# Kernel optimization log

Hardware: AMD Instinct MI355X
Metric: run time of the kernel (lower is better)

The kernel has to match this reference:

```python
import jax, jax.numpy as jnp
import numpy as np

D_MODEL = 1024
D_STATE = 128
SEQ_LEN = 4096
BATCH = 4
N_FFT = 2 ** int(np.ceil(np.log2(2 * SEQ_LEN - 1)))  # 8192
LN_EPS = 1e-3  # keras LayerNormalization default epsilon


def setup_inputs() -> dict:
    key = jax.random.key(0)
    ks = jax.random.split(key, 12)
    def dense_w(k, fan_in, fan_out):
        lim = np.sqrt(6.0 / (fan_in + fan_out)).astype(np.float32)  # glorot uniform
        return jax.random.uniform(k, (fan_in, fan_out), jnp.float32, -lim, lim)
    return {
        "x": jax.random.normal(ks[0], (BATCH, SEQ_LEN, D_MODEL), jnp.float32),
        "ln_gamma": jnp.ones((D_MODEL,), jnp.float32),
        "ln_beta": jnp.zeros((D_MODEL,), jnp.float32),
        "W_in": dense_w(ks[1], D_MODEL, D_MODEL),
        "b_in": jnp.zeros((D_MODEL,), jnp.float32),
        "W_xs": dense_w(ks[2], D_MODEL, D_STATE),
        "W_B": dense_w(ks[3], D_MODEL, D_STATE),
        "b_B": jnp.zeros((D_STATE,), jnp.float32),
        "W_C": dense_w(ks[4], D_MODEL, D_STATE),
        "b_C": jnp.zeros((D_STATE,), jnp.float32),
        "A_log": jax.random.uniform(ks[5], (D_STATE,), jnp.float32, -4.0, -1.0),
        "D": jnp.ones((D_MODEL,), jnp.float32),
        "W_so": dense_w(ks[6], D_STATE, D_MODEL),
        "W_out": dense_w(ks[7], D_MODEL, D_MODEL),
        "b_out": jnp.zeros((D_MODEL,), jnp.float32),
    }


def reference(x, ln_gamma, ln_beta, W_in, b_in, W_xs, W_B, b_B, W_C, b_C,
              A_log, D, W_so, W_out, b_out):
    residual = x
    # LayerNorm over last dim
    mu = jnp.mean(x, axis=-1, keepdims=True)
    var = jnp.mean(jnp.square(x - mu), axis=-1, keepdims=True)
    xn = (x - mu) * jax.lax.rsqrt(var + LN_EPS) * ln_gamma + ln_beta
    # projections
    z = xn @ W_in + b_in                      # [B, L, d_model]
    x_state = z @ W_xs                        # [B, L, d_state]
    B_sel = z @ W_B + b_B                     # [B, L, d_state]
    C_sel = z @ W_C + b_C                     # [B, L, d_state]
    # stable A-parameterization -> kernel K[t, s] = exp(A_s * t)
    A = -jnp.exp(A_log)                       # [d_state]
    t = jnp.arange(SEQ_LEN, dtype=jnp.float32)
    K = jnp.exp(t[:, None] * A[None, :])      # [L, d_state]
    # FFT convolution along time axis (zero-padded to N_FFT, causal slice)
    u = x_state * B_sel                       # [B, L, d_state]
    u_f = jnp.fft.rfft(u, n=N_FFT, axis=1)    # [B, N_FFT//2+1, d_state]
    k_f = jnp.fft.rfft(K, n=N_FFT, axis=0)    # [N_FFT//2+1, d_state]
    y_state = jnp.fft.irfft(u_f * k_f[None], n=N_FFT, axis=1)[:, :SEQ_LEN]
    y_state = y_state * C_sel
    # output path with skip connection through D
    y = y_state @ W_so + D * z                # [B, L, d_model]
    y = y @ W_out + b_out
    return y + residual
```

## Files before the change

### kernel.cpp

```cpp
#include <hip/hip_runtime.h>
#include <math.h>

#define D_MODEL 1024
#define D_STATE 128
#define SEQ_LEN 4096
#define BATCH 4
#define NTOK (BATCH * SEQ_LEN)
#define LN_EPS 1e-3f
#define NCHUNK 128
#define LCHUNK (SEQ_LEN / NCHUNK)

typedef __attribute__((ext_vector_type(8))) short bf16x8;
typedef __attribute__((ext_vector_type(4))) float f32x4;

__device__ __forceinline__ short f2bf(float f) {
    union { float f; unsigned u; } v; v.f = f;
    unsigned r = v.u + 0x7FFFu + ((v.u >> 16) & 1u);
    return (short)(r >> 16);
}
__device__ __forceinline__ float bf2f(short s) {
    union { unsigned u; float f; } v; v.u = ((unsigned)(unsigned short)s) << 16;
    return v.f;
}

__global__ __launch_bounds__(256) void ln_kernel(const float* __restrict__ x,
                                                 const float* __restrict__ gamma,
                                                 const float* __restrict__ beta,
                                                 short* __restrict__ xn_bf) {
    int row = blockIdx.x;
    const float4* xr = (const float4*)(x + (size_t)row * D_MODEL);
    float4 v = xr[threadIdx.x];
    float s1 = v.x + v.y + v.z + v.w;
    float s2 = v.x * v.x + v.y * v.y + v.z * v.z + v.w * v.w;
    for (int off = 32; off; off >>= 1) {
        s1 += __shfl_down(s1, off);
        s2 += __shfl_down(s2, off);
    }
    __shared__ float ls1[4], ls2[4];
    int wid = threadIdx.x >> 6, lane = threadIdx.x & 63;
    if (lane == 0) { ls1[wid] = s1; ls2[wid] = s2; }
    __syncthreads();
    s1 = ls1[0] + ls1[1] + ls1[2] + ls1[3];
    s2 = ls2[0] + ls2[1] + ls2[2] + ls2[3];
    float mu = s1 * (1.0f / D_MODEL);
    float var = s2 * (1.0f / D_MODEL) - mu * mu;
    float r = rsqrtf(var + LN_EPS);
    float4 g = ((const float4*)gamma)[threadIdx.x];
    float4 b = ((const float4*)beta)[threadIdx.x];
    short4 o;
    o.x = f2bf((v.x - mu) * r * g.x + b.x);
    o.y = f2bf((v.y - mu) * r * g.y + b.y);
    o.z = f2bf((v.z - mu) * r * g.z + b.z);
    o.w = f2bf((v.w - mu) * r * g.w + b.w);
    ((short4*)(xn_bf + (size_t)row * D_MODEL))[threadIdx.x] = o;
}

__global__ __launch_bounds__(256) void prep_kernel(
    const float* __restrict__ W_in, const float* __restrict__ W_xs,
    const float* __restrict__ W_B, const float* __restrict__ W_C,
    const float* __restrict__ W_so, const float* __restrict__ W_out,
    const float* __restrict__ bB, const float* __restrict__ bC,
    short* __restrict__ W_inT, short* __restrict__ W3T,
    short* __restrict__ W_soT, short* __restrict__ W_outT,
    float* __restrict__ bias3) {
    int blk = blockIdx.x;
    const float* in; short* out; int K, N, tile;
    if (blk < 1024)      { in = W_in;  out = W_inT;           K = 1024; N = 1024; tile = blk; }
    else if (blk < 1152) { in = W_xs;  out = W3T;             K = 1024; N = 128;  tile = blk - 1024; }
    else if (blk < 1280) { in = W_B;   out = W3T + 128*1024;  K = 1024; N = 128;  tile = blk - 1152; }
    else if (blk < 1408) { in = W_C;   out = W3T + 256*1024;  K = 1024; N = 128;  tile = blk - 1280; }
    else if (blk < 1536) { in = W_so;  out = W_soT;           K = 128;  N = 1024; tile = blk - 1408; }
    else if (blk < 2560) { in = W_out; out = W_outT;          K = 1024; N = 1024; tile = blk - 1536; }
    else {
        int t = threadIdx.y * 32 + threadIdx.x;
        for (int n = t; n < 384; n += 256)
            bias3[n] = (n < 128) ? 0.f : ((n < 256) ? bB[n - 128] : bC[n - 256]);
        return;
    }
    __shared__ float t32[32][33];
    int ntiles = N / 32;
    int nb = (tile % ntiles) * 32, kb = (tile / ntiles) * 32;
    int tx = threadIdx.x, ty = threadIdx.y;
#pragma unroll
    for (int i = 0; i < 4; ++i)
        t32[ty + 8 * i][tx] = in[(size_t)(kb + ty + 8 * i) * N + nb + tx];
    __syncthreads();
#pragma unroll
    for (int i = 0; i < 4; ++i)
        out[(size_t)(nb + ty + 8 * i) * K + kb + tx] = f2bf(t32[tx][ty + 8 * i]);
}

template<int HAS_BIAS, int HAS_ADD, int ADD_BF, int HAS_SCALE, int OUT_F32, int OUT_BF, int SWZ>
__global__ __launch_bounds__(256, 4) void gemm_bf16(
    const short* __restrict__ A, const short* __restrict__ BT,
    const float* __restrict__ bias,
    const float* __restrict__ addf, const short* __restrict__ addb,
    const float* __restrict__ addscale,
    float* __restrict__ Cf, short* __restrict__ Cbf,
    int Mt, int Nt, int K) {
    __shared__ short As[128 * 64];
    __shared__ short Bs[128 * 64];
    int p = blockIdx.x;
    int mtile, ntile;
    if (SWZ) {
        int k = p & 7, q = p >> 3;
        ntile = q & 7;
        mtile = k + 8 * (q >> 3);
    } else {
        mtile = p % Mt;
        ntile = p / Mt;
    }
    int m0 = mtile * 128, n0 = ntile * 128;
    int N = Nt * 128;
    int tid = threadIdx.x;
    int lane = tid & 63;
    int w = tid >> 6;
    int quad = lane >> 4, r16 = lane & 15;
    int wm = (w & 1) * 64, wn = (w >> 1) * 64;

    f32x4 acc[4][4] = {};

    for (int k0 = 0; k0 < K; k0 += 64) {
#pragma unroll
        for (int it = 0; it < 4; ++it) {
            int seg = it * 256 + tid;
            int row = seg >> 3, slot = seg & 7;
            int kc8 = slot ^ (row & 7);
            const short* gp = A + (size_t)(m0 + row) * K + k0 + kc8 * 8;
            __builtin_amdgcn_global_load_lds(
                (const __attribute__((address_space(1))) unsigned*)gp,
                (__attribute__((address_space(3))) unsigned*)(As + seg * 8), 16, 0, 0);
        }
#pragma unroll
        for (int it = 0; it < 4; ++it) {
            int seg = it * 256 + tid;
            int row = seg >> 3, slot = seg & 7;
            int kc8 = slot ^ (row & 7);
            const short* gp = BT + (size_t)(n0 + row) * K + k0 + kc8 * 8;
            __builtin_amdgcn_global_load_lds(
                (const __attribute__((address_space(1))) unsigned*)gp,
                (__attribute__((address_space(3))) unsigned*)(Bs + seg * 8), 16, 0, 0);
        }
        __syncthreads();

        const short* abase = As + (wm + r16) * 64;
        const short* bbase = Bs + (wn + r16) * 64;
        int sw = r16 & 7;
#pragma unroll
        for (int kk = 0; kk < 2; ++kk) {
            int phys = ((quad + 4 * kk) ^ sw) * 8;
            bf16x8 af[4], bfr[4];
#pragma unroll
            for (int i = 0; i < 4; ++i) af[i] = *(const bf16x8*)(abase + i * 16 * 64 + phys);
#pragma unroll
            for (int j = 0; j < 4; ++j) bfr[j] = *(const bf16x8*)(bbase + j * 16 * 64 + phys);
#pragma unroll
            for (int i = 0; i < 4; ++i)
#pragma unroll
                for (int j = 0; j < 4; ++j)
                    acc[i][j] = __builtin_amdgcn_mfma_f32_16x16x32_bf16(af[i], bfr[j], acc[i][j], 0, 0, 0);
        }
        __syncthreads();
    }

#pragma unroll
    for (int i = 0; i < 4; ++i) {
#pragma unroll
        for (int j = 0; j < 4; ++j) {
            int col = n0 + wn + j * 16 + r16;
            float bv = HAS_BIAS ? bias[col] : 0.f;
            float sc = HAS_SCALE ? addscale[col] : 1.f;
#pragma unroll
            for (int pr = 0; pr < 4; ++pr) {
                int row = m0 + wm + i * 16 + quad * 4 + pr;
                float v = acc[i][j][pr] + bv;
                if (HAS_ADD) {
                    float av = ADD_BF ? bf2f(addb[(size_t)row * N + col])
                                      : addf[(size_t)row * N + col];
                    v += sc * av;
                }
                if (OUT_F32) Cf[(size_t)row * N + col] = v;
                if (OUT_BF) Cbf[(size_t)row * N + col] = f2bf(v);
            }
        }
    }
}

#define WAITV8 asm volatile("s_waitcnt vmcnt(8)" ::: "memory")
#define WAITV4 asm volatile("s_waitcnt vmcnt(4)" ::: "memory")
#define WAITV0 asm volatile("s_waitcnt vmcnt(0)" ::: "memory")
#define SBARF  do { __builtin_amdgcn_s_barrier(); asm volatile("" ::: "memory"); } while (0)

template<int HAS_BIAS, int HAS_ADD, int OUT_F32, int OUT_BF, int SWZ>
__global__ __launch_bounds__(512, 2) void gemm256(
    const short* __restrict__ A, const short* __restrict__ BT,
    const float* __restrict__ bias, const float* __restrict__ addf,
    float* __restrict__ Cf, short* __restrict__ Cbf,
    int Mt, int Nt, int K) {
    __shared__ short LA[2][2][8192];
    __shared__ short LB[2][2][8192];
    int p = blockIdx.x;
    int mtile, ntile;
    if (SWZ) {
        int xcd = p & 7, q = p >> 3;
        ntile = q % Nt;
        mtile = xcd + 8 * (q / Nt);
    } else {
        mtile = p % Mt;
        ntile = p / Mt;
    }
    int m0 = mtile * 256, n0 = ntile * 256;
    int N = Nt * 256;
    int tid = threadIdx.x;
    int lane = tid & 63, w = tid >> 6;
    int quad = lane >> 4, r16 = lane & 15;
    int wm = w & 1, wn = w >> 1;
    int nt = K >> 6;

    f32x4 acc[8][4] = {};

#define STG(TU, KK, ISB) do { \
        const short* g_ = (ISB) ? BT : A; \
        int rb_ = (ISB) ? n0 : m0; \
        short* l_ = (ISB) ? &LB[(TU) & 1][KK][0] : &LA[(TU) & 1][KK][0]; \
        _Pragma("unroll") \
        for (int r_ = 0; r_ < 2; ++r_) { \
            int seg_ = r_ * 512 + tid; \
            int row_ = seg_ >> 2, sl_ = seg_ & 3; \
            int kc_ = sl_ ^ ((row_ >> 1) & 3); \
            const short* gp_ = g_ + (size_t)(rb_ + row_) * K + (TU) * 64 + (KK) * 32 + kc_ * 8; \
            __builtin_amdgcn_global_load_lds( \
                (const __attribute__((address_space(1))) unsigned*)gp_, \
                (__attribute__((address_space(3))) unsigned*)(&l_[seg_ * 8]), 16, 0, 0); \
        } \
    } while (0)

#define PH_LOADB(Bb) { _Pragma("unroll") for (int j_ = 0; j_ < 4; ++j_) \
        bf[j_] = *(const bf16x8*)((Bb) + j_ * 512 + ph4); }
#define PH_LOADA(Ab, IH) { _Pragma("unroll") for (int i_ = 0; i_ < 4; ++i_) \
        af[i_] = *(const bf16x8*)((Ab) + (i_ + 4 * (IH)) * 512 + ph4); }
#define PH_MFMA(IH) { __builtin_amdgcn_s_setprio(1); \
        _Pragma("unroll") for (int i_ = 0; i_ < 4; ++i_) \
        _Pragma("unroll") for (int j_ = 0; j_ < 4; ++j_) \
            acc[i_ + 4 * (IH)][j_] = __builtin_amdgcn_mfma_f32_16x16x32_bf16( \
                af[i_], bf[j_], acc[i_ + 4 * (IH)][j_], 0, 0, 0); \
        __builtin_amdgcn_s_setprio(0); }

    STG(0, 0, 0); STG(0, 0, 1); STG(0, 1, 0); STG(0, 1, 1); STG(1, 0, 0);

    int ph4 = (quad ^ ((r16 >> 1) & 3)) * 8;
    int arow = (wm << 7) + r16;
    int brow = (wn << 6) + r16;
    bf16x8 af[4], bf[4];

    for (int t = 0; t + 1 < nt; ++t) {
        int c = t & 1;
        const short* Ab0 = &LA[c][0][arow * 32];
        const short* Bb0 = &LB[c][0][brow * 32];
        const short* Ab1 = &LA[c][1][arow * 32];
        const short* Bb1 = &LB[c][1][brow * 32];
        STG(t + 1, 0, 1);
        WAITV8; SBARF;
        PH_LOADB(Bb0); PH_LOADA(Ab0, 0); PH_MFMA(0);
        STG(t + 1, 1, 0);
        WAITV8; SBARF;
        PH_LOADA(Ab0, 1); PH_MFMA(1);
        STG(t + 1, 1, 1);
        WAITV8; SBARF;
        PH_LOADB(Bb1); PH_LOADA(Ab1, 0); PH_MFMA(0);
        if (t + 2 < nt) STG(t + 2, 0, 0);
        WAITV8; SBARF;
        PH_LOADA(Ab1, 1); PH_MFMA(1);
    }
    {
        int c = (nt - 1) & 1;
        const short* Ab0 = &LA[c][0][arow * 32];
        const short* Bb0 = &LB[c][0][brow * 32];
        const short* Ab1 = &LA[c][1][arow * 32];
        const short* Bb1 = &LB[c][1][brow * 32];
        WAITV4; SBARF;
        PH_LOADB(Bb0); PH_LOADA(Ab0, 0); PH_MFMA(0);
        PH_LOADA(Ab0, 1); PH_MFMA(1);
        WAITV0; SBARF;
        PH_LOADB(Bb1); PH_LOADA(Ab1, 0); PH_MFMA(0);
        PH_LOADA(Ab1, 1); PH_MFMA(1);
    }
#undef STG
#undef PH_LOADB
#undef PH_LOADA
#undef PH_MFMA

#pragma unroll
    for (int i = 0; i < 8; ++i) {
#pragma unroll
        for (int j = 0; j < 4; ++j) {
            int col = n0 + wn * 64 + j * 16 + r16;
            float bv = HAS_BIAS ? bias[col] : 0.f;
#pragma unroll
            for (int pr = 0; pr < 4; ++pr) {
                int row = m0 + wm * 128 + i * 16 + quad * 4 + pr;
                float v = acc[i][j][pr] + bv;
                if (HAS_ADD) v += addf[(size_t)row * N + col];
                if (OUT_F32) Cf[(size_t)row * N + col] = v;
                if (OUT_BF) Cbf[(size_t)row * N + col] = f2bf(v);
            }
        }
    }
}

__global__ __launch_bounds__(128) void scan_p1(const float* __restrict__ s3,
                                               const float* __restrict__ A_log,
                                               float* __restrict__ hbuf,
                                               float* __restrict__ Ebuf) {
    int s = threadIdx.x;
    int c = blockIdx.x, b = blockIdx.y;
    float a = expf(-expf(A_log[s]));
    float h = 0.f;
    size_t base = (size_t)b * SEQ_LEN + (size_t)c * LCHUNK;
#pragma unroll 8
    for (int i = 0; i < LCHUNK; ++i) {
        size_t r = base + i;
        float u = s3[r * 384 + s] * s3[r * 384 + 128 + s];
        h = a * h + u;
        hbuf[r * 128 + s] = h;
    }
    Ebuf[((size_t)b * NCHUNK + c) * 128 + s] = h;
}

__global__ __launch_bounds__(512) void scan_p2(const float* __restrict__ A_log,
                                               const float* __restrict__ Ebuf,
                                               float* __restrict__ Gbuf) {
    int tid = threadIdx.x;
    int b = tid >> 7, s = tid & 127;
    float pw = expf(-expf(A_log[s]) * (float)LCHUNK);
    float G = 0.f;
    for (int c0 = 0; c0 < NCHUNK; c0 += 16) {
        float e[16];
#pragma unroll
        for (int t = 0; t < 16; ++t)
            e[t] = Ebuf[((size_t)b * NCHUNK + c0 + t) * 128 + s];
#pragma unroll
        for (int t = 0; t < 16; ++t) {
            G = pw * G + e[t];
            Gbuf[((size_t)b * NCHUNK + c0 + t) * 128 + s] = G;
        }
    }
}

__global__ __launch_bounds__(128) void scan_p3(const float* __restrict__ s3,
                                               const float* __restrict__ A_log,
                                               const float* __restrict__ hbuf,
                                               const float* __restrict__ Gbuf,
                                               short* __restrict__ ys_bf) {
    int s = threadIdx.x;
    int c = blockIdx.x, b = blockIdx.y;
    float a = expf(-expf(A_log[s]));
    float carry = (c == 0) ? 0.f : Gbuf[((size_t)b * NCHUNK + c - 1) * 128 + s];
    float p = a;
    size_t base = (size_t)b * SEQ_LEN + (size_t)c * LCHUNK;
#pragma unroll 8
    for (int i = 0; i < LCHUNK; ++i) {
        size_t r = base + i;
        float h = hbuf[r * 128 + s] + p * carry;
        p *= a;
        ys_bf[r * 128 + s] = f2bf(h * s3[r * 384 + 256 + s]);
    }
}

extern "C" void kernel_launch(void* const* d_in, const int* in_sizes, int n_in,
                              void* d_out, int out_size, void* d_ws, size_t ws_size,
                              hipStream_t stream) {
    const float* x     = (const float*)d_in[0];
    const float* ln_g  = (const float*)d_in[1];
    const float* ln_b  = (const float*)d_in[2];
    const float* W_in  = (const float*)d_in[3];
    const float* b_in  = (const float*)d_in[4];
    const float* W_xs  = (const float*)d_in[5];
    const float* W_B   = (const float*)d_in[6];
    const float* b_B   = (const float*)d_in[7];
    const float* W_C   = (const float*)d_in[8];
    const float* b_C   = (const float*)d_in[9];
    const float* A_log = (const float*)d_in[10];
    const float* Dvec  = (const float*)d_in[11];
    const float* W_so  = (const float*)d_in[12];
    const float* W_out = (const float*)d_in[13];
    const float* b_out = (const float*)d_in[14];
    float* out = (float*)d_out;

    char* w = (char*)d_ws;
    size_t off = 0;
    short* xn_bf = (short*)(w + off);
    float* hbuf  = (float*)(w + off);
    short* ys_bf = (short*)(w + off + 8388608);
    off += (size_t)NTOK * D_MODEL * 2;
    short* z_bf  = (short*)(w + off);
    off += (size_t)NTOK * D_MODEL * 2;
    short* y1_bf = (short*)(w + off);
    off += (size_t)NTOK * D_MODEL * 2;
    float* s3    = (float*)(w + off); off += (size_t)NTOK * 384 * 4;
    float* Ebuf  = (float*)(w + off); off += (size_t)BATCH * NCHUNK * 128 * 4;
    float* Gbuf  = (float*)(w + off); off += (size_t)BATCH * NCHUNK * 128 * 4;
    short* W_inT  = (short*)(w + off); off += (size_t)D_MODEL * D_MODEL * 2;
    short* W3T    = (short*)(w + off); off += (size_t)384 * D_MODEL * 2;
    short* W_soT  = (short*)(w + off); off += (size_t)D_MODEL * D_STATE * 2;
    short* W_outT = (short*)(w + off); off += (size_t)D_MODEL * D_MODEL * 2;
    float* bias3  = (float*)(w + off); off += 2048;

    prep_kernel<<<2561, dim3(32, 8), 0, stream>>>(W_in, W_xs, W_B, W_C, W_so, W_out,
                                                  b_B, b_C, W_inT, W3T, W_soT, W_outT, bias3);

    ln_kernel<<<NTOK, 256, 0, stream>>>(x, ln_g, ln_b, xn_bf);

    const int Mt = NTOK / 128;
    const int Mt2 = NTOK / 256;

    gemm256<1, 0, 0, 1, 1><<<Mt2 * 4, 512, 0, stream>>>(
        xn_bf, W_inT, b_in, nullptr, nullptr, z_bf, Mt2, 4, D_MODEL);

    gemm_bf16<1, 0, 0, 0, 1, 0, 0><<<Mt * 3, 256, 0, stream>>>(
        z_bf, W3T, bias3, nullptr, nullptr, nullptr,
        s3, nullptr, Mt, 3, D_MODEL);

    scan_p1<<<dim3(NCHUNK, BATCH), 128, 0, stream>>>(s3, A_log, hbuf, Ebuf);
    scan_p2<<<1, 512, 0, stream>>>(A_log, Ebuf, Gbuf);
    scan_p3<<<dim3(NCHUNK, BATCH), 128, 0, stream>>>(s3, A_log, hbuf, Gbuf, ys_bf);

    gemm_bf16<0, 1, 1, 1, 0, 1, 1><<<Mt * 8, 256, 0, stream>>>(
        ys_bf, W_soT, nullptr, nullptr, z_bf, Dvec,
        nullptr, y1_bf, Mt, 8, D_STATE);

    gemm256<1, 1, 1, 0, 1><<<Mt2 * 4, 512, 0, stream>>>(
        y1_bf, W_outT, b_out, x, out, nullptr, Mt2, 4, D_MODEL);
}
```

Measured before the change: 297.4 us.

## Restructure GEMM main loop into ping-pong phases with deeper global-to-LDS prefetch

Reworks the bf16 MFMA GEMM mainloop so that LDS fragment reads and the async global-to-LDS stage for a later k-tile are issued before a barrier, followed by the MFMA block and another barrier. Prefetch depth grows from about one sub-stage ahead to a full k-tile ahead, with explicit prologue and two epilogue iterations. The aim is to overlap memory traffic with MFMA work in a ping-pong style across waves and hide global latency better. It doubles the barrier count per phase, which may add synchronization overhead, and the buffer-reuse correctness depends on wait counts.

```diff
diff --git a/kernel.cpp b/kernel.cpp
--- a/kernel.cpp
+++ b/kernel.cpp
@@ -235,60 +235,65 @@
         } \
     } while (0)
 
-#define PH_LOADB(Bb) { _Pragma("unroll") for (int j_ = 0; j_ < 4; ++j_) \
-        bf[j_] = *(const bf16x8*)((Bb) + j_ * 512 + ph4); }
-#define PH_LOADA(Ab, IH) { _Pragma("unroll") for (int i_ = 0; i_ < 4; ++i_) \
-        af[i_] = *(const bf16x8*)((Ab) + (i_ + 4 * (IH)) * 512 + ph4); }
-#define PH_MFMA(IH) { __builtin_amdgcn_s_setprio(1); \
+#define RD_B(c, KK) { const short* Bb_ = &LB[c][KK][brow * 32]; \
+        _Pragma("unroll") for (int j_ = 0; j_ < 4; ++j_) \
+            bf[j_] = *(const bf16x8*)(Bb_ + j_ * 512 + ph4); }
+#define RD_A(c, KK, IH) { const short* Ab_ = &LA[c][KK][arow * 32]; \
+        _Pragma("unroll") for (int i_ = 0; i_ < 4; ++i_) \
+            af[i_] = *(const bf16x8*)(Ab_ + (i_ + 4 * (IH)) * 512 + ph4); }
+#define MM(IH) { __builtin_amdgcn_s_setprio(1); \
         _Pragma("unroll") for (int i_ = 0; i_ < 4; ++i_) \
         _Pragma("unroll") for (int j_ = 0; j_ < 4; ++j_) \
             acc[i_ + 4 * (IH)][j_] = __builtin_amdgcn_mfma_f32_16x16x32_bf16( \
                 af[i_], bf[j_], acc[i_ + 4 * (IH)][j_], 0, 0, 0); \
         __builtin_amdgcn_s_setprio(0); }
 
-    STG(0, 0, 0); STG(0, 0, 1); STG(0, 1, 0); STG(0, 1, 1); STG(1, 0, 0);
-
     int ph4 = (quad ^ ((r16 >> 1) & 3)) * 8;
     int arow = (wm << 7) + r16;
     int brow = (wn << 6) + r16;
     bf16x8 af[4], bf[4];
 
-    for (int t = 0; t + 1 < nt; ++t) {
+    STG(0, 0, 0); STG(0, 0, 1); STG(0, 1, 0); STG(0, 1, 1);
+    STG(1, 0, 0); STG(1, 0, 1);
+    WAITV8; SBARF;
+
+    for (int t = 0; t + 2 < nt; ++t) {
         int c = t & 1;
-        const short* Ab0 = &LA[c][0][arow * 32];
-        const short* Bb0 = &LB[c][0][brow * 32];
-        const short* Ab1 = &LA[c][1][arow * 32];
-        const short* Bb1 = &LB[c][1][brow * 32];
-        STG(t + 1, 0, 1);
-        WAITV8; SBARF;
-        PH_LOADB(Bb0); PH_LOADA(Ab0, 0); PH_MFMA(0);
-        STG(t + 1, 1, 0);
-        WAITV8; SBARF;
-        PH_LOADA(Ab0, 1); PH_MFMA(1);
-        STG(t + 1, 1, 1);
-        WAITV8; SBARF;
-        PH_LOADB(Bb1); PH_LOADA(Ab1, 0); PH_MFMA(0);
-        if (t + 2 < nt) STG(t + 2, 0, 0);
-        WAITV8; SBARF;
-        PH_LOADA(Ab1, 1); PH_MFMA(1);
+        RD_B(c, 0); RD_A(c, 0, 0); STG(t + 1, 1, 0);
+        SBARF; MM(0); SBARF;
+        RD_A(c, 0, 1); STG(t + 1, 1, 1); WAITV8;
+        SBARF; MM(1); SBARF;
+        RD_B(c, 1); RD_A(c, 1, 0); STG(t + 2, 0, 0);
+        SBARF; MM(0); SBARF;
+        RD_A(c, 1, 1); STG(t + 2, 0, 1); WAITV8;
+        SBARF; MM(1); SBARF;
+    }
+    {
+        int c = (nt - 2) & 1;
+        RD_B(c, 0); RD_A(c, 0, 0); STG(nt - 1, 1, 0);
+        SBARF; MM(0); SBARF;
+        RD_A(c, 0, 1); STG(nt - 1, 1, 1); WAITV8;
+        SBARF; MM(1); SBARF;
+        RD_B(c, 1); RD_A(c, 1, 0);
+        SBARF; MM(0); SBARF;
+        RD_A(c, 1, 1); WAITV4;
+        SBARF; MM(1); SBARF;
     }
     {
         int c = (nt - 1) & 1;
-        const short* Ab0 = &LA[c][0][arow * 32];
-        const short* Bb0 = &LB[c][0][brow * 32];
-        const short* Ab1 = &LA[c][1][arow * 32];
-        const short* Bb1 = &LB[c][1][brow * 32];
-        WAITV4; SBARF;
-        PH_LOADB(Bb0); PH_LOADA(Ab0, 0); PH_MFMA(0);
-        PH_LOADA(Ab0, 1); PH_MFMA(1);
-        WAITV0; SBARF;
-        PH_LOADB(Bb1); PH_LOADA(Ab1, 0); PH_MFMA(0);
-        PH_LOADA(Ab1, 1); PH_MFMA(1);
+        RD_B(c, 0); RD_A(c, 0, 0);
+        SBARF; MM(0); SBARF;
+        RD_A(c, 0, 1); WAITV0;
+        SBARF; MM(1); SBARF;
+        RD_B(c, 1); RD_A(c, 1, 0);
+        SBARF; MM(0); SBARF;
+        RD_A(c, 1, 1);
+        SBARF; MM(1);
     }
 #undef STG
-#undef PH_LOADB
-#undef PH_LOADA
-#undef PH_MFMA
+#undef RD_B
+#undef RD_A
+#undef MM
 
 #pragma unroll
     for (int i = 0; i < 8; ++i) {
```

Result: no change. 293.9 us (-1.2%).
